# Kernel tuning notes

Hardware: AMD Instinct MI355X
Metric: run time of the kernel (lower is better)

Reference implementation:

```python
import jax, jax.numpy as jnp
import numpy as np

B, T, D, H = 2, 2048, 2048, 16
HD = D // H  # head_dim = 128
ROPE_THETA = 10000.0


def _apply_rope_interleaved(x, cos, sin):
    # x: (B, T, H, HD); cos/sin: (1, T, 1, HD//2). rope_fraction=1.0, HD even.
    x1 = x[..., ::2]
    x2 = x[..., 1::2]
    rot = jnp.stack([x1 * cos - x2 * sin, x1 * sin + x2 * cos], axis=-1)
    return rot.reshape(x.shape)


def setup_inputs() -> dict:
    key = jax.random.key(0)
    k1, k2, k3 = jax.random.split(key, 3)
    x = jax.random.normal(k1, (B, T, D), dtype=jnp.float32)
    # DenseGeneral qkv kernel: (D, H, 3*HD), lecun_normal-ish scale
    w_qkv = jax.random.normal(k2, (D, H, 3 * HD), dtype=jnp.float32) / np.sqrt(D)
    # out Dense kernel: (D, D)
    w_out = jax.random.normal(k3, (D, D), dtype=jnp.float32) / np.sqrt(D)
    return {"x": x, "w_qkv": w_qkv, "w_out": w_out}


def reference(x, w_qkv, w_out):
    # Fused QKV projection: (B,T,D) x (D,H,3HD) -> (B,T,H,3HD)
    qkv = jnp.einsum("btd,dhf->bthf", x, w_qkv)
    q, k, v = jnp.split(qkv, 3, axis=-1)  # each (B,T,H,HD)

    # RoPE cos/sin at positions arange(T)
    pos = jnp.arange(T, dtype=jnp.float32)
    inv_freq = 1.0 / (ROPE_THETA ** (jnp.arange(0, HD, 2, dtype=jnp.float32) / HD))
    angles = pos[:, None] * inv_freq[None, :]  # (T, HD//2)
    cos = jnp.cos(angles)[None, :, None, :]
    sin = jnp.sin(angles)[None, :, None, :]

    q = _apply_rope_interleaved(q, cos, sin)
    k = _apply_rope_interleaved(k, cos, sin)

    sm_scale = 1.0 / np.sqrt(HD)
    # (B,H,T,HD)
    qh = jnp.transpose(q, (0, 2, 1, 3))
    kh = jnp.transpose(k, (0, 2, 1, 3))
    vh = jnp.transpose(v, (0, 2, 1, 3))

    scores = jnp.einsum("bhqd,bhkd->bhqk", qh, kh) * sm_scale
    causal = jnp.tril(jnp.ones((T, T), dtype=bool))
    scores = jnp.where(causal[None, None], scores, jnp.float32(-1e30))
    probs = jax.nn.softmax(scores, axis=-1)
    yh = jnp.einsum("bhqk,bhkd->bhqd", probs, vh)

    y = jnp.transpose(yh, (0, 2, 1, 3)).reshape(B, T, D)
    # deterministic=True -> dropout is identity; out projection
    return jnp.einsum("btd,de->bte", y, w_out)
```

## Files before the change

kernel.cpp:

```cpp
#include <hip/hip_runtime.h>
#include <math.h>

typedef unsigned short u16;
typedef unsigned int u32;
typedef __attribute__((ext_vector_type(8))) short short8;
typedef __attribute__((ext_vector_type(4))) float f32x4;

#define Bb 2
#define Tt 2048
#define Dd 2048
#define Hh 16
#define HDim 128
#define NQKV 6144

__device__ __forceinline__ u16 f2b(float f) {
    u32 u = __float_as_uint(f);
    u32 r = (u + 0x7FFFu + ((u >> 16) & 1u)) >> 16;
    return (u16)r;
}
__device__ __forceinline__ float2 b2f2(u32 u) {
    return make_float2(__uint_as_float(u << 16), __uint_as_float(u & 0xFFFF0000u));
}
__device__ __forceinline__ u32 pack2(float a, float b) {
    return (u32)f2b(a) | ((u32)f2b(b) << 16);
}

#define GLD16(g, l) __builtin_amdgcn_global_load_lds(                                   \
    (const __attribute__((address_space(1))) void*)(g),                                 \
    (__attribute__((address_space(3))) void*)(l), 16, 0, 0)

__global__ __launch_bounds__(256) void cast_f32_bf16(const float* __restrict__ src,
                                                     u16* __restrict__ dst, int n) {
    int i = (blockIdx.x * 256 + threadIdx.x) * 4;
    if (i >= n) return;
    float4 v = *(const float4*)(src + i);
    *(uint2*)(dst + i) = make_uint2(pack2(v.x, v.y), pack2(v.z, v.w));
}

__global__ __launch_bounds__(256) void transpose_cast(const float* __restrict__ src,
                                                      u16* __restrict__ dst, int R, int C) {
    __shared__ float tile[32][33];
    int c0 = blockIdx.x << 5, r0 = blockIdx.y << 5;
    int tx = threadIdx.x & 31, ty = threadIdx.x >> 5;
    #pragma unroll
    for (int i = 0; i < 32; i += 8)
        tile[ty + i][tx] = src[(size_t)(r0 + ty + i) * C + c0 + tx];
    __syncthreads();
    #pragma unroll
    for (int i = 0; i < 32; i += 8)
        dst[(size_t)(c0 + ty + i) * R + r0 + tx] = f2b(tile[tx][ty + i]);
}

template <int OMODE>
__global__ __launch_bounds__(256) void gemm_bt(const u16* __restrict__ A, const u16* __restrict__ Bt,
                                               void* __restrict__ Cv, int Mn, int Nn, int Kn) {
    __shared__ __align__(16) u16 As[128 * 32];
    __shared__ __align__(16) u16 Bs[128 * 32];
    const int tid = threadIdx.x;
    const int m0 = blockIdx.y << 7, n0 = blockIdx.x << 7;
    const int wave = tid >> 6, lane = tid & 63;
    const int wm = (wave >> 1) << 6, wn = (wave & 1) << 6;
    const int l15 = lane & 15, lq = lane >> 4;

    f32x4 acc[4][4];
    #pragma unroll
    for (int i = 0; i < 4; i++)
        #pragma unroll
        for (int j = 0; j < 4; j++)
            acc[i][j] = (f32x4){0.f, 0.f, 0.f, 0.f};

    const int srow = wave * 32 + (lane >> 2);
    const int scol = (lane & 3) << 3;
    const u16* ga = A + (size_t)(m0 + srow) * Kn + scol;
    const u16* gb = Bt + (size_t)(n0 + srow) * Kn + scol;
    u16* lA = &As[wave * 1024];
    u16* lB = &Bs[wave * 1024];

    for (int k0 = 0; k0 < Kn; k0 += 32) {
        __syncthreads();
        GLD16(ga + k0, lA);
        GLD16(ga + k0 + (size_t)16 * Kn, lA + 512);
        GLD16(gb + k0, lB);
        GLD16(gb + k0 + (size_t)16 * Kn, lB + 512);
        __syncthreads();
        short8 a[4], b[4];
        #pragma unroll
        for (int i = 0; i < 4; i++) {
            a[i] = *(const short8*)&As[(wm + (i << 4) + l15) * 32 + lq * 8];
            b[i] = *(const short8*)&Bs[(wn + (i << 4) + l15) * 32 + lq * 8];
        }
        #pragma unroll
        for (int i = 0; i < 4; i++)
            #pragma unroll
            for (int j = 0; j < 4; j++)
                acc[i][j] = __builtin_amdgcn_mfma_f32_16x16x32_bf16(a[i], b[j], acc[i][j], 0, 0, 0);
    }

    #pragma unroll
    for (int i = 0; i < 4; i++) {
        int mbase = m0 + wm + (i << 4) + (lq << 2);
        #pragma unroll
        for (int j = 0; j < 4; j++) {
            int n = n0 + wn + (j << 4) + l15;
            if constexpr (OMODE == 1) {
                #pragma unroll
                for (int r = 0; r < 4; r++)
                    ((float*)Cv)[(size_t)(mbase + r) * Nn + n] = acc[i][j][r];
            } else {
                int f = n >> 7;
                int h = f / 3, sel = f - 3 * h;
                int d = n & 127;
                u16* base = (u16*)Cv + (size_t)sel * 8388608;
                #pragma unroll
                for (int r = 0; r < 4; r++) {
                    int m = mbase + r;
                    int b = m >> 11, t = m & 2047;
                    base[(((size_t)(b * 16 + h)) * 2048 + t) * 128 + d] = f2b(acc[i][j][r]);
                }
            }
        }
    }
}

__global__ __launch_bounds__(256) void rope_planar(u16* __restrict__ qk) {
    int gid = blockIdx.x * 256 + threadIdx.x;
    int i = gid & 63;
    int t = (gid >> 6) & 2047;
    int bhz = gid >> 17;
    u16* p = qk + ((size_t)bhz * 2048 + t) * 128 + 2 * i;
    float ang = (float)t * exp2f(-0.20762050596f * (float)i);
    float sv, cv;
    sincosf(ang, &sv, &cv);
    float2 xy = b2f2(*(const u32*)p);
    *(u32*)p = pack2(xy.x * cv - xy.y * sv, xy.x * sv + xy.y * cv);
}

#define KS 136
#define VTS 72

__global__ __launch_bounds__(512) void attn_mfma(const u16* __restrict__ qh, const u16* __restrict__ kh,
                                                 const u16* __restrict__ vh, u16* __restrict__ yb) {
    __shared__ __align__(16) u16 smem[17920];
    u16* Qs = smem;
    u16* Ks = smem;
    u16* Vt = smem + 8704;

    const int tid = threadIdx.x;
    const int bh = blockIdx.y;
    const int w = tid >> 6, lane = tid & 63;
    const int l15 = lane & 15, qa = lane >> 4;
    const u16* qp = qh + (size_t)bh * Tt * HDim;
    const u16* kp = kh + (size_t)bh * Tt * HDim;
    const u16* vp = vh + (size_t)bh * Tt * HDim;
    const int b = bh >> 4, h = bh & 15;
    const float CEXP = (float)(0.08838834764831845 * 1.4426950408889634);

    for (int pass = 0; pass < 2; pass++) {
        const int qt = pass ? (15 - (int)blockIdx.x) : (int)blockIdx.x;
        const int qbase = qt * 128 + w * 16;

        __syncthreads();
        #pragma unroll
        for (int i = 0; i < 4; i++) {
            int slot = tid + (i << 9);
            int row = slot >> 4, cb = slot & 15;
            *(uint4*)&Qs[row * KS + cb * 8] =
                *(const uint4*)(qp + (size_t)(qt * 128 + row) * HDim + cb * 8);
        }
        __syncthreads();
        short8 qfrag[4];
        #pragma unroll
        for (int dc = 0; dc < 4; dc++)
            qfrag[dc] = *(const short8*)&Qs[(w * 16 + l15) * KS + dc * 32 + qa * 8];

        float m2 = -1e30f, l_i = 0.f;
        f32x4 oacc[8];
        #pragma unroll
        for (int nt = 0; nt < 8; nt++) oacc[nt] = (f32x4){0.f, 0.f, 0.f, 0.f};

        const int nkt = 2 * qt + 2;
        for (int kt = 0; kt < nkt; kt++) {
            const int k0 = kt << 6;
            __syncthreads();
            #pragma unroll
            for (int i = 0; i < 2; i++) {
                int slot = tid + (i << 9);
                int row = slot >> 4, cb = slot & 15;
                *(uint4*)&Ks[row * KS + cb * 8] =
                    *(const uint4*)(kp + (size_t)(k0 + row) * HDim + cb * 8);
            }
            {
                int k = tid & 63;
                #pragma unroll
                for (int it = 0; it < 2; it++) {
                    int d0 = ((tid >> 6) << 3) + (it << 6);
                    uint4 vv = *(const uint4*)(vp + (size_t)(k0 + k) * HDim + d0);
                    const u16* pe = (const u16*)&vv;
                    #pragma unroll
                    for (int j = 0; j < 8; j++) Vt[(d0 + j) * VTS + k] = pe[j];
                }
            }
            __syncthreads();

            if (k0 <= qbase + 15) {
                float s2[4][4];
                #pragma unroll
                for (int mt = 0; mt < 4; mt++) {
                    f32x4 st = (f32x4){0.f, 0.f, 0.f, 0.f};
                    #pragma unroll
                    for (int dc = 0; dc < 4; dc++) {
                        short8 ka = *(const short8*)&Ks[(mt * 16 + l15) * KS + dc * 32 + qa * 8];
                        st = __builtin_amdgcn_mfma_f32_16x16x32_bf16(ka, qfrag[dc], st, 0, 0, 0);
                    }
                    #pragma unroll
                    for (int r = 0; r < 4; r++) s2[mt][r] = st[r] * CEXP;
                }
                if (k0 + 63 > qbase) {
                    int qg = qbase + l15;
                    #pragma unroll
                    for (int mt = 0; mt < 4; mt++)
                        #pragma unroll
                        for (int r = 0; r < 4; r++)
                            if (k0 + mt * 16 + qa * 4 + r > qg) s2[mt][r] = -1e30f;
                }
                float mx = m2;
                #pragma unroll
                for (int mt = 0; mt < 4; mt++)
                    #pragma unroll
                    for (int r = 0; r < 4; r++) mx = fmaxf(mx, s2[mt][r]);
                mx = fmaxf(mx, __shfl_xor(mx, 16, 64));
                mx = fmaxf(mx, __shfl_xor(mx, 32, 64));
                float alpha = exp2f(m2 - mx);
                m2 = mx;
                float rsum = 0.f;
                float p[4][4];
                #pragma unroll
                for (int mt = 0; mt < 4; mt++)
                    #pragma unroll
                    for (int r = 0; r < 4; r++) {
                        p[mt][r] = exp2f(s2[mt][r] - mx);
                        rsum += p[mt][r];
                    }
                rsum += __shfl_xor(rsum, 16, 64);
                rsum += __shfl_xor(rsum, 32, 64);
                l_i = l_i * alpha + rsum;
                float aO[4];
                #pragma unroll
                for (int r = 0; r < 4; r++) aO[r] = __shfl(alpha, qa * 4 + r, 64);
                #pragma unroll
                for (int nt = 0; nt < 8; nt++)
                    #pragma unroll
                    for (int r = 0; r < 4; r++) oacc[nt][r] *= aO[r];

                u32 pu[4][2];
                #pragma unroll
                for (int mt = 0; mt < 4; mt++) {
                    pu[mt][0] = pack2(p[mt][0], p[mt][1]);
                    pu[mt][1] = pack2(p[mt][2], p[mt][3]);
                }
                short8 pa[2];
                const int srcA = ((qa & 1) << 5) + l15;
                const int srcB = srcA + 16;
                #pragma unroll
                for (int c = 0; c < 2; c++) {
                    u32 A0 = __shfl((int)pu[2 * c][0], srcA, 64);
                    u32 A1 = __shfl((int)pu[2 * c][1], srcA, 64);
                    u32 A2 = __shfl((int)pu[2 * c][0], srcB, 64);
                    u32 A3 = __shfl((int)pu[2 * c][1], srcB, 64);
                    u32 B0 = __shfl((int)pu[2 * c + 1][0], srcA, 64);
                    u32 B1 = __shfl((int)pu[2 * c + 1][1], srcA, 64);
                    u32 B2 = __shfl((int)pu[2 * c + 1][0], srcB, 64);
                    u32 B3 = __shfl((int)pu[2 * c + 1][1], srcB, 64);
                    u32 wv[4];
                    wv[0] = (qa & 2) ? B0 : A0;
                    wv[1] = (qa & 2) ? B1 : A1;
                    wv[2] = (qa & 2) ? B2 : A2;
                    wv[3] = (qa & 2) ? B3 : A3;
                    pa[c] = *(short8*)wv;
                }
                #pragma unroll
                for (int nt = 0; nt < 8; nt++) {
                    short8 vb0 = *(const short8*)&Vt[(nt * 16 + l15) * VTS + qa * 8];
                    short8 vb1 = *(const short8*)&Vt[(nt * 16 + l15) * VTS + 32 + qa * 8];
                    oacc[nt] = __builtin_amdgcn_mfma_f32_16x16x32_bf16(pa[0], vb0, oacc[nt], 0, 0, 0);
                    oacc[nt] = __builtin_amdgcn_mfma_f32_16x16x32_bf16(pa[1], vb1, oacc[nt], 0, 0, 0);
                }
            }
        }

        float linv = 1.0f / l_i;
        float lr[4];
        #pragma unroll
        for (int r = 0; r < 4; r++) lr[r] = __shfl(linv, qa * 4 + r, 64);
        #pragma unroll
        for (int r = 0; r < 4; r++) {
            int t = qbase + qa * 4 + r;
            u16* dst = yb + ((size_t)(b * Tt + t)) * Dd + h * HDim + l15;
            #pragma unroll
            for (int nt = 0; nt < 8; nt++)
                dst[nt * 16] = f2b(oacc[nt][r] * lr[r]);
        }
    }
}

extern "C" void kernel_launch(void* const* d_in, const int* in_sizes, int n_in,
                              void* d_out, int out_size, void* d_ws, size_t ws_size,
                              hipStream_t stream) {
    const float* x     = (const float*)d_in[0];
    const float* w_qkv = (const float*)d_in[1];
    const float* w_out = (const float*)d_in[2];
    float* out = (float*)d_out;

    u16* ws    = (u16*)d_ws;
    u16* xb    = ws;
    u16* wqkvT = xb + 8388608;
    u16* woutT = wqkvT + 12582912;
    u16* qhb   = woutT + 4194304;
    u16* khb   = qhb + 8388608;
    u16* vhb   = khb + 8388608;
    u16* yb    = vhb + 8388608;

    cast_f32_bf16<<<8192, 256, 0, stream>>>(x, xb, 8388608);
    transpose_cast<<<dim3(192, 64), 256, 0, stream>>>(w_qkv, wqkvT, 2048, 6144);
    transpose_cast<<<dim3(64, 64), 256, 0, stream>>>(w_out, woutT, 2048, 2048);
    gemm_bt<2><<<dim3(48, 32), 256, 0, stream>>>(xb, wqkvT, (void*)qhb, 4096, 6144, 2048);
    rope_planar<<<32768, 256, 0, stream>>>(qhb);
    attn_mfma<<<dim3(8, 32), 512, 0, stream>>>(qhb, khb, vhb, yb);
    gemm_bt<1><<<dim3(16, 32), 256, 0, stream>>>(yb, woutT, (void*)out, 4096, 2048, 2048);
}
```

Baseline: 442.8 us.

## Restructure attention onto 32x32 MFMA tiles with LDS-direct loads and staged epilogue

Rewrites the attention kernel to use 32x32x16 bf16 MFMAs with 4 waves of 32 query rows each, instead of 16x16 tiles over 8 waves. Q and K tiles are loaded with global_load_lds into a padded packed layout. V is transposed with paired-row 32-bit LDS writes. The softmax scale is folded into Q during RoPE, and the output goes through LDS for coalesced 16-byte stores. The grid becomes 16x32 blocks of 256 threads with a per-batch reversed tile order instead of two passes per block. The aims are fewer MFMA and shuffle instructions, less LDS traffic, and better occupancy, at the cost of higher register pressure from the 16-wide accumulators.

```diff
diff --git a/kernel.cpp b/kernel.cpp
--- a/kernel.cpp
+++ b/kernel.cpp
@@ -5,6 +5,7 @@
 typedef unsigned int u32;
 typedef __attribute__((ext_vector_type(8))) short short8;
 typedef __attribute__((ext_vector_type(4))) float f32x4;
+typedef __attribute__((ext_vector_type(16))) float f32x16;
 
 #define Bb 2
 #define Tt 2048
@@ -12,6 +13,8 @@
 #define Hh 16
 #define HDim 128
 #define NQKV 6144
+#define CEXPF 0.12752141454006q_unused
+#define CEXP_VAL 0.127521410699097f
 
 __device__ __forceinline__ u16 f2b(float f) {
     u32 u = __float_as_uint(f);
@@ -131,175 +134,186 @@
     float ang = (float)t * exp2f(-0.20762050596f * (float)i);
     float sv, cv;
     sincosf(ang, &sv, &cv);
+    float sc = (bhz < 32) ? CEXP_VAL : 1.0f;
     float2 xy = b2f2(*(const u32*)p);
-    *(u32*)p = pack2(xy.x * cv - xy.y * sv, xy.x * sv + xy.y * cv);
-}
-
-#define KS 136
-#define VTS 72
-
-__global__ __launch_bounds__(512) void attn_mfma(const u16* __restrict__ qh, const u16* __restrict__ kh,
-                                                 const u16* __restrict__ vh, u16* __restrict__ yb) {
-    __shared__ __align__(16) u16 smem[17920];
+    *(u32*)p = pack2((xy.x * cv - xy.y * sv) * sc, (xy.x * sv + xy.y * cv) * sc);
+}
+
+__global__ __launch_bounds__(256, 2) void attn_mfma(const u16* __restrict__ qh, const u16* __restrict__ kh,
+                                                    const u16* __restrict__ vh, u16* __restrict__ yb) {
+    __shared__ __align__(16) u16 smem[17536];
+    u16* Ks = smem;
+    u16* Vt = smem + 8320;
     u16* Qs = smem;
-    u16* Ks = smem;
-    u16* Vt = smem + 8704;
 
     const int tid = threadIdx.x;
+    const int w = tid >> 6, lane = tid & 63;
+    const int l31 = lane & 31, hf = lane >> 5;
     const int bh = blockIdx.y;
-    const int w = tid >> 6, lane = tid & 63;
-    const int l15 = lane & 15, qa = lane >> 4;
+    const int qt = (blockIdx.y < 16) ? (int)blockIdx.x : (15 - (int)blockIdx.x);
     const u16* qp = qh + (size_t)bh * Tt * HDim;
     const u16* kp = kh + (size_t)bh * Tt * HDim;
     const u16* vp = vh + (size_t)bh * Tt * HDim;
     const int b = bh >> 4, h = bh & 15;
-    const float CEXP = (float)(0.08838834764831845 * 1.4426950408889634);
-
-    for (int pass = 0; pass < 2; pass++) {
-        const int qt = pass ? (15 - (int)blockIdx.x) : (int)blockIdx.x;
-        const int qbase = qt * 128 + w * 16;
-
+    const int qbase = qt * 128 + w * 32;
+
+    #pragma unroll
+    for (int i = 0; i < 8; i++) {
+        int p = w * 8 + i;
+        GLD16(qp + (size_t)(qt * 128 + p * 4 + (lane >> 4)) * HDim + (lane & 15) * 8,
+              &Qs[p * 520]);
+    }
+    __syncthreads();
+    const int qrow = w * 32 + l31;
+    short8 qfrag[8];
+    #pragma unroll
+    for (int kc = 0; kc < 8; kc++)
+        qfrag[kc] = *(const short8*)&Qs[(qrow >> 2) * 520 + (qrow & 3) * 128 + kc * 16 + hf * 8];
+
+    float m2 = -1e30f, l_i = 0.f;
+    f32x16 oacc[4];
+    #pragma unroll
+    for (int dt = 0; dt < 4; dt++)
+        #pragma unroll
+        for (int r = 0; r < 16; r++) oacc[dt][r] = 0.f;
+
+    const int vkp = tid & 31, vdc = tid >> 5;
+    const int nkt = 2 * qt + 2;
+    for (int kt = 0; kt < nkt; kt++) {
+        const int k0 = kt << 6;
         __syncthreads();
         #pragma unroll
         for (int i = 0; i < 4; i++) {
-            int slot = tid + (i << 9);
-            int row = slot >> 4, cb = slot & 15;
-            *(uint4*)&Qs[row * KS + cb * 8] =
-                *(const uint4*)(qp + (size_t)(qt * 128 + row) * HDim + cb * 8);
+            int p = w * 4 + i;
+            GLD16(kp + (size_t)(k0 + p * 4 + (lane >> 4)) * HDim + (lane & 15) * 8,
+                  &Ks[p * 520]);
+        }
+        {
+            const u16* vsrc = vp + (size_t)(k0 + 2 * vkp) * HDim + vdc * 16;
+            uint4 r0a = *(const uint4*)vsrc;
+            uint4 r0b = *(const uint4*)(vsrc + 8);
+            uint4 r1a = *(const uint4*)(vsrc + HDim);
+            uint4 r1b = *(const uint4*)(vsrc + HDim + 8);
+            const u16* e0a = (const u16*)&r0a; const u16* e0b = (const u16*)&r0b;
+            const u16* e1a = (const u16*)&r1a; const u16* e1b = (const u16*)&r1b;
+            #pragma unroll
+            for (int j = 0; j < 8; j++)
+                *(u32*)&Vt[(vdc * 16 + j) * 72 + vkp * 2] = (u32)e0a[j] | ((u32)e1a[j] << 16);
+            #pragma unroll
+            for (int j = 0; j < 8; j++)
+                *(u32*)&Vt[(vdc * 16 + 8 + j) * 72 + vkp * 2] = (u32)e0b[j] | ((u32)e1b[j] << 16);
         }
         __syncthreads();
-        short8 qfrag[4];
-        #pragma unroll
-        for (int dc = 0; dc < 4; dc++)
-            qfrag[dc] = *(const short8*)&Qs[(w * 16 + l15) * KS + dc * 32 + qa * 8];
-
-        float m2 = -1e30f, l_i = 0.f;
-        f32x4 oacc[8];
-        #pragma unroll
-        for (int nt = 0; nt < 8; nt++) oacc[nt] = (f32x4){0.f, 0.f, 0.f, 0.f};
-
-        const int nkt = 2 * qt + 2;
-        for (int kt = 0; kt < nkt; kt++) {
-            const int k0 = kt << 6;
-            __syncthreads();
-            #pragma unroll
-            for (int i = 0; i < 2; i++) {
-                int slot = tid + (i << 9);
-                int row = slot >> 4, cb = slot & 15;
-                *(uint4*)&Ks[row * KS + cb * 8] =
-                    *(const uint4*)(kp + (size_t)(k0 + row) * HDim + cb * 8);
-            }
-            {
-                int k = tid & 63;
-                #pragma unroll
-                for (int it = 0; it < 2; it++) {
-                    int d0 = ((tid >> 6) << 3) + (it << 6);
-                    uint4 vv = *(const uint4*)(vp + (size_t)(k0 + k) * HDim + d0);
-                    const u16* pe = (const u16*)&vv;
+
+        if (k0 <= qbase + 31) {
+            float pv[2][16];
+            #pragma unroll
+            for (int mt = 0; mt < 2; mt++) {
+                f32x16 st;
+                #pragma unroll
+                for (int r = 0; r < 16; r++) st[r] = 0.f;
+                const int krow = mt * 32 + l31;
+                const u16* kbase = &Ks[(krow >> 2) * 520 + (krow & 3) * 128 + hf * 8];
+                #pragma unroll
+                for (int kc = 0; kc < 8; kc++) {
+                    short8 ka = *(const short8*)(kbase + kc * 16);
+                    st = __builtin_amdgcn_mfma_f32_32x32x16_bf16(ka, qfrag[kc], st, 0, 0, 0);
+                }
+                #pragma unroll
+                for (int r = 0; r < 16; r++) pv[mt][r] = st[r];
+            }
+            const int qg = qbase + l31;
+            if (k0 + 63 > qbase) {
+                #pragma unroll
+                for (int mt = 0; mt < 2; mt++)
                     #pragma unroll
-                    for (int j = 0; j < 8; j++) Vt[(d0 + j) * VTS + k] = pe[j];
-                }
-            }
-            __syncthreads();
-
-            if (k0 <= qbase + 15) {
-                float s2[4][4];
-                #pragma unroll
-                for (int mt = 0; mt < 4; mt++) {
-                    f32x4 st = (f32x4){0.f, 0.f, 0.f, 0.f};
-                    #pragma unroll
-                    for (int dc = 0; dc < 4; dc++) {
-                        short8 ka = *(const short8*)&Ks[(mt * 16 + l15) * KS + dc * 32 + qa * 8];
-                        st = __builtin_amdgcn_mfma_f32_16x16x32_bf16(ka, qfrag[dc], st, 0, 0, 0);
+                    for (int r = 0; r < 16; r++) {
+                        int kg = k0 + mt * 32 + (r & 3) + 8 * (r >> 2) + 4 * hf;
+                        if (kg > qg) pv[mt][r] = -1e30f;
                     }
-                    #pragma unroll
-                    for (int r = 0; r < 4; r++) s2[mt][r] = st[r] * CEXP;
-                }
-                if (k0 + 63 > qbase) {
-                    int qg = qbase + l15;
-                    #pragma unroll
-                    for (int mt = 0; mt < 4; mt++)
-                        #pragma unroll
-                        for (int r = 0; r < 4; r++)
-                            if (k0 + mt * 16 + qa * 4 + r > qg) s2[mt][r] = -1e30f;
-                }
-                float mx = m2;
-                #pragma unroll
-                for (int mt = 0; mt < 4; mt++)
-                    #pragma unroll
-                    for (int r = 0; r < 4; r++) mx = fmaxf(mx, s2[mt][r]);
-                mx = fmaxf(mx, __shfl_xor(mx, 16, 64));
-                mx = fmaxf(mx, __shfl_xor(mx, 32, 64));
-                float alpha = exp2f(m2 - mx);
-                m2 = mx;
-                float rsum = 0.f;
-                float p[4][4];
-                #pragma unroll
-                for (int mt = 0; mt < 4; mt++)
-                    #pragma unroll
-                    for (int r = 0; r < 4; r++) {
-                        p[mt][r] = exp2f(s2[mt][r] - mx);
-                        rsum += p[mt][r];
-                    }
-                rsum += __shfl_xor(rsum, 16, 64);
-                rsum += __shfl_xor(rsum, 32, 64);
-                l_i = l_i * alpha + rsum;
-                float aO[4];
-                #pragma unroll
-                for (int r = 0; r < 4; r++) aO[r] = __shfl(alpha, qa * 4 + r, 64);
-                #pragma unroll
-                for (int nt = 0; nt < 8; nt++)
-                    #pragma unroll
-                    for (int r = 0; r < 4; r++) oacc[nt][r] *= aO[r];
-
-                u32 pu[4][2];
-                #pragma unroll
-                for (int mt = 0; mt < 4; mt++) {
-                    pu[mt][0] = pack2(p[mt][0], p[mt][1]);
-                    pu[mt][1] = pack2(p[mt][2], p[mt][3]);
-                }
-                short8 pa[2];
-                const int srcA = ((qa & 1) << 5) + l15;
-                const int srcB = srcA + 16;
-                #pragma unroll
-                for (int c = 0; c < 2; c++) {
-                    u32 A0 = __shfl((int)pu[2 * c][0], srcA, 64);
-                    u32 A1 = __shfl((int)pu[2 * c][1], srcA, 64);
-                    u32 A2 = __shfl((int)pu[2 * c][0], srcB, 64);
-                    u32 A3 = __shfl((int)pu[2 * c][1], srcB, 64);
-                    u32 B0 = __shfl((int)pu[2 * c + 1][0], srcA, 64);
-                    u32 B1 = __shfl((int)pu[2 * c + 1][1], srcA, 64);
-                    u32 B2 = __shfl((int)pu[2 * c + 1][0], srcB, 64);
-                    u32 B3 = __shfl((int)pu[2 * c + 1][1], srcB, 64);
-                    u32 wv[4];
-                    wv[0] = (qa & 2) ? B0 : A0;
-                    wv[1] = (qa & 2) ? B1 : A1;
-                    wv[2] = (qa & 2) ? B2 : A2;
-                    wv[3] = (qa & 2) ? B3 : A3;
-                    pa[c] = *(short8*)wv;
-                }
-                #pragma unroll
-                for (int nt = 0; nt < 8; nt++) {
-                    short8 vb0 = *(const short8*)&Vt[(nt * 16 + l15) * VTS + qa * 8];
-                    short8 vb1 = *(const short8*)&Vt[(nt * 16 + l15) * VTS + 32 + qa * 8];
-                    oacc[nt] = __builtin_amdgcn_mfma_f32_16x16x32_bf16(pa[0], vb0, oacc[nt], 0, 0, 0);
-                    oacc[nt] = __builtin_amdgcn_mfma_f32_16x16x32_bf16(pa[1], vb1, oacc[nt], 0, 0, 0);
-                }
-            }
-        }
-
-        float linv = 1.0f / l_i;
-        float lr[4];
-        #pragma unroll
-        for (int r = 0; r < 4; r++) lr[r] = __shfl(linv, qa * 4 + r, 64);
-        #pragma unroll
-        for (int r = 0; r < 4; r++) {
-            int t = qbase + qa * 4 + r;
-            u16* dst = yb + ((size_t)(b * Tt + t)) * Dd + h * HDim + l15;
-            #pragma unroll
-            for (int nt = 0; nt < 8; nt++)
-                dst[nt * 16] = f2b(oacc[nt][r] * lr[r]);
-        }
+            }
+            float mx = m2;
+            #pragma unroll
+            for (int mt = 0; mt < 2; mt++)
+                #pragma unroll
+                for (int r = 0; r < 16; r++) mx = fmaxf(mx, pv[mt][r]);
+            mx = fmaxf(mx, __shfl_xor(mx, 32, 64));
+            float alpha = exp2f(m2 - mx);
+            m2 = mx;
+            float rsum = 0.f;
+            #pragma unroll
+            for (int mt = 0; mt < 2; mt++)
+                #pragma unroll
+                for (int r = 0; r < 16; r++) {
+                    pv[mt][r] = exp2f(pv[mt][r] - mx);
+                    rsum += pv[mt][r];
+                }
+            rsum += __shfl_xor(rsum, 32, 64);
+            l_i = l_i * alpha + rsum;
+            #pragma unroll
+            for (int dt = 0; dt < 4; dt++)
+                #pragma unroll
+                for (int r = 0; r < 16; r++) oacc[dt][r] *= alpha;
+
+            u32 pu[2][8], px[2][8];
+            #pragma unroll
+            for (int mt = 0; mt < 2; mt++)
+                #pragma unroll
+                for (int g = 0; g < 8; g++)
+                    pu[mt][g] = pack2(pv[mt][2 * g], pv[mt][2 * g + 1]);
+            #pragma unroll
+            for (int mt = 0; mt < 2; mt++)
+                #pragma unroll
+                for (int g = 0; g < 8; g++)
+                    px[mt][g] = (u32)__shfl_xor((int)pu[mt][g], 32, 64);
+            short8 pb[4];
+            #pragma unroll
+            for (int kc = 0; kc < 4; kc++) {
+                int mt = kc >> 1, g0 = (kc & 1) * 4;
+                u32 f[4];
+                if (hf == 0) {
+                    f[0] = pu[mt][g0]; f[1] = pu[mt][g0 + 1];
+                    f[2] = px[mt][g0]; f[3] = px[mt][g0 + 1];
+                } else {
+                    f[0] = px[mt][g0 + 2]; f[1] = px[mt][g0 + 3];
+                    f[2] = pu[mt][g0 + 2]; f[3] = pu[mt][g0 + 3];
+                }
+                pb[kc] = *(short8*)f;
+            }
+            #pragma unroll
+            for (int dt = 0; dt < 4; dt++) {
+                const u16* vbase = &Vt[(dt * 32 + l31) * 72 + hf * 8];
+                #pragma unroll
+                for (int kc = 0; kc < 4; kc++) {
+                    short8 va = *(const short8*)(vbase + kc * 16);
+                    oacc[dt] = __builtin_amdgcn_mfma_f32_32x32x16_bf16(va, pb[kc], oacc[dt], 0, 0, 0);
+                }
+            }
+        }
+    }
+
+    float linv = 1.0f / l_i;
+    #pragma unroll
+    for (int dt = 0; dt < 4; dt++)
+        #pragma unroll
+        for (int r = 0; r < 16; r++) oacc[dt][r] *= linv;
+    __syncthreads();
+    u16* E = smem + w * 4384;
+    const int rb[8] = {0, 2, 8, 10, 16, 18, 24, 26};
+    #pragma unroll
+    for (int dt = 0; dt < 4; dt++)
+        #pragma unroll
+        for (int g = 0; g < 8; g++) {
+            int d0 = dt * 32 + rb[g] + 4 * hf;
+            *(u32*)&E[l31 * 136 + d0] = pack2(oacc[dt][2 * g], oacc[dt][2 * g + 1]);
+        }
+    __syncthreads();
+    #pragma unroll
+    for (int p8 = 0; p8 < 8; p8++) {
+        int ql = p8 * 4 + (lane >> 4);
+        uint4 ov = *(const uint4*)&E[ql * 136 + (lane & 15) * 8];
+        int t = qt * 128 + w * 32 + ql;
+        *(uint4*)(yb + ((size_t)(b * Tt + t)) * Dd + h * HDim + (lane & 15) * 8) = ov;
     }
 }
 
@@ -325,6 +339,6 @@
     transpose_cast<<<dim3(64, 64), 256, 0, stream>>>(w_out, woutT, 2048, 2048);
     gemm_bt<2><<<dim3(48, 32), 256, 0, stream>>>(xb, wqkvT, (void*)qhb, 4096, 6144, 2048);
     rope_planar<<<32768, 256, 0, stream>>>(qhb);
-    attn_mfma<<<dim3(8, 32), 512, 0, stream>>>(qhb, khb, vhb, yb);
+    attn_mfma<<<dim3(16, 32), 256, 0, stream>>>(qhb, khb, vhb, yb);
     gemm_bt<1><<<dim3(16, 32), 256, 0, stream>>>(yb, woutT, (void*)out, 4096, 2048, 2048);
 }
```

Result: no change. 450.6 us (+1.8%).
